# Kernel optimization log

Measured on AMD Instinct MI355X. Metric: run time of the kernel, lower is better.

## Reference

```python
import jax, jax.numpy as jnp
import numpy as np

DECAY = 0.9
THRESHOLD = 1.0


def setup_inputs() -> dict:
    key = jax.random.key(0)
    k1, k2 = jax.random.split(key)
    B, T, I, N = 128, 512, 1024, 1024
    x = jax.random.normal(k1, (B, T, I), dtype=jnp.float32)
    weights = jax.random.uniform(k2, (N, I), dtype=jnp.float32)  # torch.rand init
    return {"x": x, "weights": weights}


def reference(x, weights):
    # x: [B, T, I], weights: [N, I]
    # Hoist the matmul out of the time loop: currents[t] == weights @ x[:, t, :].T
    currents = jnp.einsum("ni,bti->tnb", weights, x)  # [T, N, B]

    def step(mp, i_t):
        mp = DECAY * mp + i_t
        spike_mask = (mp >= THRESHOLD).astype(mp.dtype)
        mp = mp * (1.0 - spike_mask)  # reset fired neurons
        return mp, spike_mask

    mp0 = jnp.zeros((weights.shape[0], x.shape[0]), dtype=x.dtype)  # [N, B]
    _, masks = jax.lax.scan(step, mp0, currents)
    return masks.sum(axis=0)  # spikes: [N, B]
```

## Files before the change

### kernel.cpp

```cpp
#include <hip/hip_runtime.h>
#include <stdint.h>

#define T_DIM 512
#define B_DIM 128
#define I_DIM 1024
#define N_DIM 1024
#define NB (N_DIM * B_DIM)
#define ROWB 4096

#define DECAY 0.9f
#define THRESH 1.0f

typedef _Float16 f16;
typedef _Float16 f16x8 __attribute__((ext_vector_type(8)));
typedef float f32x4 __attribute__((ext_vector_type(4)));

__global__ __launch_bounds__(256) void split_w_kernel(
    const float* __restrict__ W, f16* __restrict__ Ws)
{
    int gid = blockIdx.x * 256 + threadIdx.x;
    int kc  = gid & 127;
    int row = gid >> 7;
    const float* src = W + (size_t)row * I_DIM + kc * 8;
    f16* dst = Ws + (size_t)row * 2048 + kc * 16;
    float v[8];
    *(float4*)&v[0] = *(const float4*)src;
    *(float4*)&v[4] = *(const float4*)(src + 4);
    f16 hi[8], lo[8];
    #pragma unroll
    for (int j = 0; j < 8; ++j) {
        hi[j] = (f16)v[j];
        lo[j] = (f16)(v[j] - (float)hi[j]);
    }
    *(f16x8*)dst       = *(const f16x8*)hi;
    *(f16x8*)(dst + 8) = *(const f16x8*)lo;
}

__global__ __launch_bounds__(512, 2) void spk_gemm_kernel(
    const uint8_t* __restrict__ Wsb,
    const float* __restrict__ X,
    float* __restrict__ C,
    int t0, int tc)
{
    __shared__ __align__(16) uint8_t lds[131072];

    const int tid  = threadIdx.x;
    const int wave = tid >> 6, lane = tid & 63;

    const int nwg = gridDim.x;
    const int q = nwg >> 3, r = nwg & 7;
    const int xcd = blockIdx.x & 7, idx = blockIdx.x >> 3;
    const int wg = (xcd < r ? xcd * (q + 1) : r * (q + 1) + (xcd - r) * q) + idx;
    const int n0    = (wg & 3) << 8;
    const int tpair = wg >> 2;
    const int tA    = t0 + tpair * 2;

    const uint8_t* srcp[8];
    #pragma unroll
    for (int c = 0; c < 8; ++c) {
        int G = c * 512 + tid;
        if (c < 4) {
            int rr = G >> 3, g = G & 7;
            int gg = g ^ (rr & 7);
            srcp[c] = Wsb + (size_t)(n0 + rr) * ROWB + gg * 16;
        } else {
            int Gb = G - 2048;
            int rr = Gb >> 3, g = Gb & 7;
            int gg = g ^ (rr & 7);
            int brow = rr & 127, tt = tA + (rr >> 7);
            srcp[c] = (const uint8_t*)X + ((size_t)brow * T_DIM + tt) * (I_DIM * 4) + gg * 16;
        }
    }

    const int wr = wave >> 2, wc = wave & 3;
    const int l15 = lane & 15, kcg = lane >> 4, l7 = l15 & 7;

    const int aBaseH = (wr * 128 + l15) * 128 + ((((kcg << 1) | 0) ^ l7) << 4);
    const int aBaseL = (wr * 128 + l15) * 128 + ((((kcg << 1) | 1) ^ l7) << 4);
    const int bBase0 = 32768 + (wc * 64 + l15) * 128 + ((((kcg << 1) | 0) ^ l7) << 4);
    const int bBase1 = 32768 + (wc * 64 + l15) * 128 + ((((kcg << 1) | 1) ^ l7) << 4);

    f32x4 acc[8][4];
    #pragma unroll
    for (int m = 0; m < 8; ++m)
        #pragma unroll
        for (int n = 0; n < 4; ++n) acc[m][n] = (f32x4){0.f, 0.f, 0.f, 0.f};

    #pragma unroll
    for (int c = 0; c < 8; ++c)
        __builtin_amdgcn_global_load_lds(
            (const __attribute__((address_space(1))) uint8_t*)srcp[c],
            (__attribute__((address_space(3))) uint8_t*)&lds[c * 8192 + wave * 1024],
            16, 0, 0);

    for (int kt = 0; kt < 32; ++kt) {
        const int buf = kt & 1;
        __builtin_amdgcn_s_barrier();
        if (kt + 1 < 32) {
            const int nb = (buf ^ 1) << 16;
            #pragma unroll
            for (int c = 0; c < 8; ++c)
                __builtin_amdgcn_global_load_lds(
                    (const __attribute__((address_space(1))) uint8_t*)(srcp[c] + (kt + 1) * 128),
                    (__attribute__((address_space(3))) uint8_t*)&lds[nb + c * 8192 + wave * 1024],
                    16, 0, 0);
            asm volatile("s_waitcnt vmcnt(8)" ::: "memory");
        } else {
            asm volatile("s_waitcnt vmcnt(0)" ::: "memory");
        }
        __builtin_amdgcn_s_barrier();
        __builtin_amdgcn_sched_barrier(0);

        const uint8_t* bp = &lds[buf << 16];

        f16x8 Ah[8], Al[8];
        #pragma unroll
        for (int m = 0; m < 8; ++m) {
            Ah[m] = *(const f16x8*)&bp[aBaseH + m * 2048];
            Al[m] = *(const f16x8*)&bp[aBaseL + m * 2048];
        }
        #pragma unroll
        for (int nf = 0; nf < 4; ++nf) {
            f32x4 b0 = *(const f32x4*)&bp[bBase0 + nf * 2048];
            f32x4 b1 = *(const f32x4*)&bp[bBase1 + nf * 2048];
            float bf[8];
            bf[0] = b0[0]; bf[1] = b0[1]; bf[2] = b0[2]; bf[3] = b0[3];
            bf[4] = b1[0]; bf[5] = b1[1]; bf[6] = b1[2]; bf[7] = b1[3];
            f16x8 Bh, Bl;
            #pragma unroll
            for (int j = 0; j < 8; ++j) {
                f16 h = (f16)bf[j];
                Bh[j] = h;
                Bl[j] = (f16)(bf[j] - (float)h);
            }
            __builtin_amdgcn_s_setprio(1);
            #pragma unroll
            for (int m = 0; m < 8; ++m) {
                acc[m][nf] = __builtin_amdgcn_mfma_f32_16x16x32_f16(Ah[m], Bh, acc[m][nf], 0, 0, 0);
                acc[m][nf] = __builtin_amdgcn_mfma_f32_16x16x32_f16(Ah[m], Bl, acc[m][nf], 0, 0, 0);
                acc[m][nf] = __builtin_amdgcn_mfma_f32_16x16x32_f16(Al[m], Bh, acc[m][nf], 0, 0, 0);
            }
            __builtin_amdgcn_s_setprio(0);
        }
    }

    const int tsub = wc >> 1, bb = (wc & 1) * 64;
    float* cp = C + (size_t)(tpair * 2 + tsub) * NB;
    const int rg = (lane >> 4) << 2;
    #pragma unroll
    for (int m = 0; m < 8; ++m) {
        int nrow = n0 + wr * 128 + m * 16 + rg;
        #pragma unroll
        for (int nf = 0; nf < 4; ++nf) {
            int col = bb + nf * 16 + l15;
            #pragma unroll
            for (int j = 0; j < 4; ++j)
                cp[(size_t)(nrow + j) * B_DIM + col] = acc[m][nf][j];
        }
    }
}

__global__ __launch_bounds__(256) void spk_scan_kernel(
    const float* __restrict__ cur,
    float* __restrict__ mp_state,
    float* __restrict__ out,
    int tc, int first)
{
    const int nb = blockIdx.x * 256 + threadIdx.x;
    float mp, cnt;
    if (first) { mp = 0.0f; cnt = 0.0f; }
    else       { mp = mp_state[nb]; cnt = out[nb]; }

    const float* p = cur + nb;
    #pragma unroll 8
    for (int t = 0; t < tc; ++t) {
        float c = p[(size_t)t * NB];
        mp = __fadd_rn(__fmul_rn(DECAY, mp), c);
        if (mp >= THRESH) { cnt += 1.0f; mp = 0.0f; }
    }
    mp_state[nb] = mp;
    out[nb] = cnt;
}

extern "C" void kernel_launch(void* const* d_in, const int* in_sizes, int n_in,
                              void* d_out, int out_size, void* d_ws, size_t ws_size,
                              hipStream_t stream) {
    const float* x = (const float*)d_in[0];
    const float* w = (const float*)d_in[1];
    float* out = (float*)d_out;

    uint8_t* ws = (uint8_t*)d_ws;
    float* mp  = (float*)ws;
    f16*   Wsp = (f16*)(ws + 524288);
    uint8_t* rest = ws + 524288 + 4194304;
    size_t rem = ws_size - 524288 - 4194304;

    int Tc = (int)(rem / (size_t)(NB * 4));
    if (Tc > T_DIM) Tc = T_DIM;
    Tc &= ~1;
    if (Tc < 2) Tc = 2;

    float* cur = (float*)rest;

    split_w_kernel<<<(N_DIM * I_DIM / 8) / 256, 256, 0, stream>>>(w, Wsp);

    int first = 1;
    for (int t0 = 0; t0 < T_DIM; ) {
        int tc = T_DIM - t0;
        if (tc > Tc) tc = Tc;

        spk_gemm_kernel<<<(tc / 2) * 4, 512, 0, stream>>>(
            (const uint8_t*)Wsp, x, cur, t0, tc);
        spk_scan_kernel<<<NB / 256, 256, 0, stream>>>(cur, mp, out, tc, first);

        first = 0;
        t0 += tc;
    }
}
```

Baseline: 503.7 us.

## Shrink GEMM workgroup tile to 128x128 per timestep with 256 threads

The GEMM workgroup goes from a 256-row by 256-column tile (two timesteps, 8 waves, 128 KB LDS) to a 128x128 tile for a single timestep with 4 waves and 64 KB LDS. The MFMA inner loop is reordered so all B fragments are converted up front and the three split-precision passes are issued as grouped 4x4 batches. The aim is higher occupancy and more workgroups for load balance. In exchange, each loaded W and X tile is reused less, so global and LDS traffic per FLOP rises.

```diff
diff --git a/kernel.cpp b/kernel.cpp
--- a/kernel.cpp
+++ b/kernel.cpp
@@ -36,13 +36,13 @@
     *(f16x8*)(dst + 8) = *(const f16x8*)lo;
 }
 
-__global__ __launch_bounds__(512, 2) void spk_gemm_kernel(
+__global__ __launch_bounds__(256, 2) void spk_gemm_kernel(
     const uint8_t* __restrict__ Wsb,
     const float* __restrict__ X,
     float* __restrict__ C,
-    int t0, int tc)
+    int t0)
 {
-    __shared__ __align__(16) uint8_t lds[131072];
+    __shared__ __align__(16) uint8_t lds[65536];
 
     const int tid  = threadIdx.x;
     const int wave = tid >> 6, lane = tid & 63;
@@ -51,38 +51,42 @@
     const int q = nwg >> 3, r = nwg & 7;
     const int xcd = blockIdx.x & 7, idx = blockIdx.x >> 3;
     const int wg = (xcd < r ? xcd * (q + 1) : r * (q + 1) + (xcd - r) * q) + idx;
-    const int n0    = (wg & 3) << 8;
-    const int tpair = wg >> 2;
-    const int tA    = t0 + tpair * 2;
+    const int n0 = (wg & 7) << 7;
+    const int t  = t0 + (wg >> 3);
 
     const uint8_t* srcp[8];
     #pragma unroll
     for (int c = 0; c < 8; ++c) {
-        int G = c * 512 + tid;
         if (c < 4) {
+            int G = c * 256 + tid;
             int rr = G >> 3, g = G & 7;
-            int gg = g ^ (rr & 7);
-            srcp[c] = Wsb + (size_t)(n0 + rr) * ROWB + gg * 16;
+            srcp[c] = Wsb + (size_t)(n0 + rr) * ROWB + ((g ^ (rr & 7)) << 4);
         } else {
-            int Gb = G - 2048;
-            int rr = Gb >> 3, g = Gb & 7;
-            int gg = g ^ (rr & 7);
-            int brow = rr & 127, tt = tA + (rr >> 7);
-            srcp[c] = (const uint8_t*)X + ((size_t)brow * T_DIM + tt) * (I_DIM * 4) + gg * 16;
-        }
-    }
-
-    const int wr = wave >> 2, wc = wave & 3;
+            int G = (c - 4) * 256 + tid;
+            int rr = G >> 3, g = G & 7;
+            srcp[c] = (const uint8_t*)X + ((size_t)rr * T_DIM + t) * (I_DIM * 4)
+                      + ((g ^ (rr & 7)) << 4);
+        }
+    }
+
+    const int wr = ((wave >> 1) << 6);
+    const int wc = ((wave & 1) << 6);
     const int l15 = lane & 15, kcg = lane >> 4, l7 = l15 & 7;
 
-    const int aBaseH = (wr * 128 + l15) * 128 + ((((kcg << 1) | 0) ^ l7) << 4);
-    const int aBaseL = (wr * 128 + l15) * 128 + ((((kcg << 1) | 1) ^ l7) << 4);
-    const int bBase0 = 32768 + (wc * 64 + l15) * 128 + ((((kcg << 1) | 0) ^ l7) << 4);
-    const int bBase1 = 32768 + (wc * 64 + l15) * 128 + ((((kcg << 1) | 1) ^ l7) << 4);
-
-    f32x4 acc[8][4];
-    #pragma unroll
-    for (int m = 0; m < 8; ++m)
+    int aoffH[4], aoffL[4], boff0[4], boff1[4];
+    #pragma unroll
+    for (int m = 0; m < 4; ++m) {
+        int ra = wr + m * 16 + l15;
+        aoffH[m] = ra * 128 + ((((kcg << 1) | 0) ^ l7) << 4);
+        aoffL[m] = ra * 128 + ((((kcg << 1) | 1) ^ l7) << 4);
+        int rb = wc + m * 16 + l15;
+        boff0[m] = 16384 + rb * 128 + (((kcg * 2 + 0) ^ l7) << 4);
+        boff1[m] = 16384 + rb * 128 + (((kcg * 2 + 1) ^ l7) << 4);
+    }
+
+    f32x4 acc[4][4];
+    #pragma unroll
+    for (int m = 0; m < 4; ++m)
         #pragma unroll
         for (int n = 0; n < 4; ++n) acc[m][n] = (f32x4){0.f, 0.f, 0.f, 0.f};
 
@@ -90,19 +94,19 @@
     for (int c = 0; c < 8; ++c)
         __builtin_amdgcn_global_load_lds(
             (const __attribute__((address_space(1))) uint8_t*)srcp[c],
-            (__attribute__((address_space(3))) uint8_t*)&lds[c * 8192 + wave * 1024],
+            (__attribute__((address_space(3))) uint8_t*)&lds[(c * 256 + tid - lane) * 16],
             16, 0, 0);
 
     for (int kt = 0; kt < 32; ++kt) {
         const int buf = kt & 1;
         __builtin_amdgcn_s_barrier();
         if (kt + 1 < 32) {
-            const int nb = (buf ^ 1) << 16;
+            const int nb = (buf ^ 1) << 15;
             #pragma unroll
             for (int c = 0; c < 8; ++c)
                 __builtin_amdgcn_global_load_lds(
                     (const __attribute__((address_space(1))) uint8_t*)(srcp[c] + (kt + 1) * 128),
-                    (__attribute__((address_space(3))) uint8_t*)&lds[nb + c * 8192 + wave * 1024],
+                    (__attribute__((address_space(3))) uint8_t*)&lds[nb + (c * 256 + tid - lane) * 16],
                     16, 0, 0);
             asm volatile("s_waitcnt vmcnt(8)" ::: "memory");
         } else {
@@ -111,51 +115,64 @@
         __builtin_amdgcn_s_barrier();
         __builtin_amdgcn_sched_barrier(0);
 
-        const uint8_t* bp = &lds[buf << 16];
-
-        f16x8 Ah[8], Al[8];
-        #pragma unroll
-        for (int m = 0; m < 8; ++m) {
-            Ah[m] = *(const f16x8*)&bp[aBaseH + m * 2048];
-            Al[m] = *(const f16x8*)&bp[aBaseL + m * 2048];
-        }
-        #pragma unroll
-        for (int nf = 0; nf < 4; ++nf) {
-            f32x4 b0 = *(const f32x4*)&bp[bBase0 + nf * 2048];
-            f32x4 b1 = *(const f32x4*)&bp[bBase1 + nf * 2048];
+        const uint8_t* bp = &lds[buf << 15];
+
+        f32x4 b0[4], b1[4];
+        #pragma unroll
+        for (int n = 0; n < 4; ++n) {
+            b0[n] = *(const f32x4*)&bp[boff0[n]];
+            b1[n] = *(const f32x4*)&bp[boff1[n]];
+        }
+        f16x8 Ah[4], Al[4];
+        #pragma unroll
+        for (int m = 0; m < 4; ++m) {
+            Ah[m] = *(const f16x8*)&bp[aoffH[m]];
+            Al[m] = *(const f16x8*)&bp[aoffL[m]];
+        }
+        f16x8 Bh[4], Bl[4];
+        #pragma unroll
+        for (int n = 0; n < 4; ++n) {
             float bf[8];
-            bf[0] = b0[0]; bf[1] = b0[1]; bf[2] = b0[2]; bf[3] = b0[3];
-            bf[4] = b1[0]; bf[5] = b1[1]; bf[6] = b1[2]; bf[7] = b1[3];
-            f16x8 Bh, Bl;
+            bf[0] = b0[n][0]; bf[1] = b0[n][1]; bf[2] = b0[n][2]; bf[3] = b0[n][3];
+            bf[4] = b1[n][0]; bf[5] = b1[n][1]; bf[6] = b1[n][2]; bf[7] = b1[n][3];
             #pragma unroll
             for (int j = 0; j < 8; ++j) {
                 f16 h = (f16)bf[j];
-                Bh[j] = h;
-                Bl[j] = (f16)(bf[j] - (float)h);
+                Bh[n][j] = h;
+                Bl[n][j] = (f16)(bf[j] - (float)h);
             }
-            __builtin_amdgcn_s_setprio(1);
-            #pragma unroll
-            for (int m = 0; m < 8; ++m) {
-                acc[m][nf] = __builtin_amdgcn_mfma_f32_16x16x32_f16(Ah[m], Bh, acc[m][nf], 0, 0, 0);
-                acc[m][nf] = __builtin_amdgcn_mfma_f32_16x16x32_f16(Ah[m], Bl, acc[m][nf], 0, 0, 0);
-                acc[m][nf] = __builtin_amdgcn_mfma_f32_16x16x32_f16(Al[m], Bh, acc[m][nf], 0, 0, 0);
-            }
-            __builtin_amdgcn_s_setprio(0);
-        }
-    }
-
-    const int tsub = wc >> 1, bb = (wc & 1) * 64;
-    float* cp = C + (size_t)(tpair * 2 + tsub) * NB;
+        }
+
+        __builtin_amdgcn_s_setprio(1);
+        #pragma unroll
+        for (int m = 0; m < 4; ++m)
+            #pragma unroll
+            for (int n = 0; n < 4; ++n)
+                acc[m][n] = __builtin_amdgcn_mfma_f32_16x16x32_f16(Ah[m], Bh[n], acc[m][n], 0, 0, 0);
+        #pragma unroll
+        for (int m = 0; m < 4; ++m)
+            #pragma unroll
+            for (int n = 0; n < 4; ++n)
+                acc[m][n] = __builtin_amdgcn_mfma_f32_16x16x32_f16(Ah[m], Bl[n], acc[m][n], 0, 0, 0);
+        #pragma unroll
+        for (int m = 0; m < 4; ++m)
+            #pragma unroll
+            for (int n = 0; n < 4; ++n)
+                acc[m][n] = __builtin_amdgcn_mfma_f32_16x16x32_f16(Al[m], Bh[n], acc[m][n], 0, 0, 0);
+        __builtin_amdgcn_s_setprio(0);
+    }
+
+    float* cp = C + (size_t)(wg >> 3) * NB;
     const int rg = (lane >> 4) << 2;
     #pragma unroll
-    for (int m = 0; m < 8; ++m) {
-        int nrow = n0 + wr * 128 + m * 16 + rg;
-        #pragma unroll
-        for (int nf = 0; nf < 4; ++nf) {
-            int col = bb + nf * 16 + l15;
+    for (int m = 0; m < 4; ++m) {
+        int nrow = n0 + wr + m * 16 + rg;
+        #pragma unroll
+        for (int n = 0; n < 4; ++n) {
+            int col = wc + n * 16 + l15;
             #pragma unroll
             for (int j = 0; j < 4; ++j)
-                cp[(size_t)(nrow + j) * B_DIM + col] = acc[m][nf][j];
+                cp[(size_t)(nrow + j) * B_DIM + col] = acc[m][n][j];
         }
     }
 }
@@ -197,8 +214,7 @@
 
     int Tc = (int)(rem / (size_t)(NB * 4));
     if (Tc > T_DIM) Tc = T_DIM;
-    Tc &= ~1;
-    if (Tc < 2) Tc = 2;
+    if (Tc < 1) Tc = 1;
 
     float* cur = (float*)rest;
 
@@ -209,8 +225,7 @@
         int tc = T_DIM - t0;
         if (tc > Tc) tc = Tc;
 
-        spk_gemm_kernel<<<(tc / 2) * 4, 512, 0, stream>>>(
-            (const uint8_t*)Wsp, x, cur, t0, tc);
+        spk_gemm_kernel<<<tc * 8, 256, 0, stream>>>((const uint8_t*)Wsp, x, cur, t0);
         spk_scan_kernel<<<NB / 256, 256, 0, stream>>>(cur, mp, out, tc, first);
 
         first = 0;
```

After: 528.0 us. +4.8%, slower.
